# Optimization experiments

Measured on AMD Instinct MI355X. Metric: run time of the kernel, lower is better.

Reference implementation:

```python
import jax, jax.numpy as jnp
import numpy as np

B = 16384      # number of batched 6-node FC graphs
A = 6          # num_agents (nodes per graph)
D_OBS = 128    # raw observation dim
D_EMB = 250    # embedding / GAT feature dim
H = 3          # GAT heads (head outputs averaged to keep dim 250)
HID = 256
N_ACT = 5
NEG_SLOPE = 0.2


def setup_inputs() -> dict:
    key = jax.random.key(0)
    ks = jax.random.split(key, 16)
    def w(i, shape, scale=0.05):
        return jax.random.normal(ks[i], shape, dtype=jnp.float32) * scale
    return {
        "x": jax.random.normal(ks[0], (B * A, D_OBS), dtype=jnp.float32),
        "W_emb": w(1, (D_OBS, D_EMB)), "b_emb": jnp.zeros((D_EMB,), jnp.float32),
        "W_gat": w(2, (H, D_EMB, D_EMB)),
        "a_l": w(3, (H, D_EMB)), "a_r": w(4, (H, D_EMB)),
        "W1": w(5, (2 * D_EMB, HID)), "b1": jnp.zeros((HID,), jnp.float32),
        "W2": w(6, (HID, N_ACT)), "b2": jnp.zeros((N_ACT,), jnp.float32),
        "V1": w(7, (2 * D_EMB, HID)), "vb1": jnp.zeros((HID,), jnp.float32),
        "V2": w(8, (HID, 1)), "vb2": jnp.zeros((1,), jnp.float32),
    }


def reference(x, W_emb, b_emb, W_gat, a_l, a_r, W1, b1, W2, b2, V1, vb1, V2, vb2):
    # embedding layer
    h = jax.nn.relu(x @ W_emb + b_emb)                       # [N, 250]
    hb = h.reshape(B, A, D_EMB)                              # [B, 6, 250]
    # GAT on fully-connected 6-node graphs (incl. self edges), dense-masked form
    Wh = jnp.einsum("bad,hde->bhae", hb, W_gat)              # [B, H, 6, 250]
    el = jnp.einsum("bhae,he->bha", Wh, a_l)                 # dst term
    er = jnp.einsum("bhae,he->bha", Wh, a_r)                 # src term
    e = jax.nn.leaky_relu(el[:, :, :, None] + er[:, :, None, :], NEG_SLOPE)  # [B,H,6,6]
    attn = jax.nn.softmax(e, axis=-1)                        # edge softmax over neighbors
    gat = jnp.einsum("bhij,bhje->bhie", attn, Wh).mean(axis=1)  # mean over heads -> [B,6,250]
    feat = jnp.concatenate([hb, gat], axis=-1).reshape(B * A, 2 * D_EMB)  # [N, 500]
    # actor head (reg1)
    probs = jax.nn.softmax(jax.nn.relu(feat @ W1 + b1) @ W2 + b2, axis=-1)  # [N, 5]
    # critic head (reg2)
    value = jax.nn.relu(feat @ V1 + vb1) @ V2 + vb2           # [N, 1]
    return jnp.concatenate([probs, value], axis=-1)          # [N, 6]
```

## Files before the change

### kernel.cpp

```cpp
#include <hip/hip_runtime.h>

typedef unsigned short u16;
typedef unsigned int   u32;
typedef unsigned long long u64;
typedef __attribute__((ext_vector_type(4))) int   i32x4;
typedef __attribute__((ext_vector_type(4))) float f32x4;
typedef __attribute__((ext_vector_type(8))) short s16x8;

#define NROWS 98304L
#define LDF   512

__device__ __forceinline__ u16 f2bf(float x) {
  union { float f; u32 u; } v; v.f = x;
  return (u16)((v.u + 0x7FFFu + ((v.u >> 16) & 1u)) >> 16);
}
__device__ __forceinline__ float bf2f(u16 b) {
  union { float f; u32 u; } v; v.u = ((u32)b) << 16;
  return v.f;
}

__device__ __forceinline__ void gload_lds16(const u16* g, u16* l) {
  __builtin_amdgcn_global_load_lds(
      (const __attribute__((address_space(1))) unsigned int*)g,
      (__attribute__((address_space(3))) unsigned int*)l, 16, 0, 0);
}

__global__ __launch_bounds__(256)
void prep_weights(const float* __restrict__ W_emb, const float* __restrict__ b_emb,
                  const float* __restrict__ W_gat, const float* __restrict__ a_l,
                  const float* __restrict__ a_r, const float* __restrict__ W1,
                  const float* __restrict__ b1, const float* __restrict__ V1,
                  const float* __restrict__ vb1,
                  u16* __restrict__ Wemb_t, u16* __restrict__ Wgat_t,
                  u16* __restrict__ W1V1_t, float* __restrict__ bembp,
                  float* __restrict__ b1vb1)
{
  const int idx = blockIdx.x * 256 + threadIdx.x;
  const int stride = gridDim.x * 256;
  for (int t = idx; t < 256 * 128; t += stride) {
    int n = t >> 7, k = t & 127;
    Wemb_t[t] = f2bf(n < 250 ? W_emb[k * 250 + n] : 0.f);
  }
  for (int t = idx; t < 3 * 256 * 256; t += stride) {
    int h = t >> 16, rem = t & 65535, e = rem >> 8, d = rem & 255;
    float v = 0.f;
    if (e < 250 && d < 250) {
      v = W_gat[(h * 250 + d) * 250 + e];
    } else if ((e == 250 || e == 251) && d < 250) {
      const float* av = ((e == 250) ? a_l : a_r) + h * 250;
      const float* wrow = W_gat + ((long)h * 250 + d) * 250;
      float s = 0.f;
      for (int q = 0; q < 250; q++) s += wrow[q] * av[q];
      v = s;
    }
    Wgat_t[t] = f2bf(v);
  }
  for (int t = idx; t < 512 * 512; t += stride) {
    int n = t >> 9, k = t & 511;
    const float* src = (n < 256) ? W1 : V1;
    int col = n & 255;
    float v = 0.f;
    if (k < 250) v = src[k * 256 + col];
    else if (k >= 256 && k < 506) v = src[(k - 6) * 256 + col];
    W1V1_t[t] = f2bf(v);
  }
  for (int t = idx; t < 512; t += stride) b1vb1[t] = (t < 256) ? b1[t] : vb1[t - 256];
  for (int t = idx; t < 256; t += stride) bembp[t] = (t < 250) ? b_emb[t] : 0.f;
}

__global__ __launch_bounds__(256)
void cvt_x(const float* __restrict__ x, u16* __restrict__ xb)
{
  const long n = NROWS * 128;
  long i = ((long)blockIdx.x * 256 + threadIdx.x) * 8;
  const long stride = (long)gridDim.x * 256 * 8;
  for (; i < n; i += stride) {
    f32x4 a = *(const f32x4*)(x + i);
    f32x4 b = *(const f32x4*)(x + i + 4);
    i32x4 o;
    o[0] = (int)((u32)f2bf(a[0]) | ((u32)f2bf(a[1]) << 16));
    o[1] = (int)((u32)f2bf(a[2]) | ((u32)f2bf(a[3]) << 16));
    o[2] = (int)((u32)f2bf(b[0]) | ((u32)f2bf(b[1]) << 16));
    o[3] = (int)((u32)f2bf(b[2]) | ((u32)f2bf(b[3]) << 16));
    *(i32x4*)(xb + i) = o;
  }
}

template<int KSTEPS, int EPI>
__global__ __launch_bounds__(256, 2)
void gemm_bf16(const u16* __restrict__ A, int lda,
               const u16* __restrict__ B, int ldb, long strideB,
               u16* __restrict__ C, int ldc, long strideC,
               const float* __restrict__ bias)
{
  __shared__ __align__(16) u16 At[128 * 64];
  __shared__ __align__(16) u16 Bt[128 * 64];
  const int tid = threadIdx.x;
  const int w = tid >> 6, lane = tid & 63;
  const int fl = lane & 15, fh = lane >> 4;
  const int wr = (w >> 1) * 64, wc = (w & 1) * 64;
  const int srow = lane >> 3;
  const int scol = (((lane & 7) ^ srow) << 3);
  const int swz = (fl & 7) << 3;

  const u16* Ab = A + (long)blockIdx.x * 128 * lda;
  const u16* Bb = B + (long)blockIdx.z * strideB + (long)blockIdx.y * 128 * ldb;
  u16* Cb = C + (long)blockIdx.z * strideC + (long)blockIdx.x * 128 * ldc + blockIdx.y * 128;
  const float* biasb = bias + blockIdx.y * 128;

  f32x4 acc[4][4];
  #pragma unroll
  for (int m = 0; m < 4; m++)
    #pragma unroll
    for (int n = 0; n < 4; n++)
      acc[m][n] = f32x4{0.f, 0.f, 0.f, 0.f};

  for (int ks = 0; ks < KSTEPS; ks++) {
    __syncthreads();
    #pragma unroll
    for (int c = 0; c < 4; c++) {
      const int row = w * 32 + c * 8 + srow;
      gload_lds16(Ab + (long)row * lda + ks * 64 + scol, At + (w * 4 + c) * 512);
      gload_lds16(Bb + (long)row * ldb + ks * 64 + scol, Bt + (w * 4 + c) * 512);
    }
    __syncthreads();
    #pragma unroll
    for (int kk = 0; kk < 2; kk++) {
      s16x8 af[4], bfr[4];
      #pragma unroll
      for (int m = 0; m < 4; m++)
        af[m] = *(const s16x8*)(At + (wr + m * 16 + fl) * 64 + ((kk * 32 + fh * 8) ^ swz));
      #pragma unroll
      for (int n = 0; n < 4; n++)
        bfr[n] = *(const s16x8*)(Bt + (wc + n * 16 + fl) * 64 + ((kk * 32 + fh * 8) ^ swz));
      #pragma unroll
      for (int m = 0; m < 4; m++)
        #pragma unroll
        for (int n = 0; n < 4; n++)
          acc[m][n] = __builtin_amdgcn_mfma_f32_16x16x32_bf16(af[m], bfr[n], acc[m][n], 0, 0, 0);
    }
  }
  #pragma unroll
  for (int m = 0; m < 4; m++) {
    const int r0 = wr + m * 16 + fh * 4;
    #pragma unroll
    for (int n = 0; n < 4; n++) {
      const int col = wc + n * 16 + fl;
      float bvv = 0.f;
      if constexpr (EPI == 1) bvv = biasb[col];
      f32x4 v = acc[m][n];
      #pragma unroll
      for (int r = 0; r < 4; r++) {
        float xv = v[r];
        if constexpr (EPI == 1) xv = fmaxf(xv + bvv, 0.f);
        Cb[(long)(r0 + r) * ldc + col] = f2bf(xv);
      }
    }
  }
}

__global__ __launch_bounds__(256)
void attn_gat(const u16* __restrict__ Wh, u16* __restrict__ feat)
{
  const int w = threadIdx.x >> 6, lane = threadIdx.x & 63;
  const long g = (long)blockIdx.x * 4 + w;
  const int c0 = lane * 4;

  u64 raw[3][6];
  #pragma unroll
  for (int h = 0; h < 3; h++)
    #pragma unroll
    for (int i = 0; i < 6; i++)
      raw[h][i] = *(const u64*)(Wh + (((long)h * NROWS + g * 6 + i) << 8) + c0);

  float gacc[6][4];
  #pragma unroll
  for (int i = 0; i < 6; i++)
    #pragma unroll
    for (int q = 0; q < 4; q++) gacc[i][q] = 0.f;

  #pragma unroll
  for (int h = 0; h < 3; h++) {
    float whf[6][4];
    #pragma unroll
    for (int i = 0; i < 6; i++) {
      u64 v = raw[h][i];
      whf[i][0] = bf2f((u16)v);
      whf[i][1] = bf2f((u16)(v >> 16));
      whf[i][2] = bf2f((u16)(v >> 32));
      whf[i][3] = bf2f((u16)(v >> 48));
    }
    float el[6], er[6];
    #pragma unroll
    for (int i = 0; i < 6; i++) {
      el[i] = __shfl(whf[i][2], 62, 64);
      er[i] = __shfl(whf[i][3], 62, 64);
    }
    #pragma unroll
    for (int i = 0; i < 6; i++) {
      float e[6]; float mx = -1e30f;
      #pragma unroll
      for (int j = 0; j < 6; j++) {
        float t = el[i] + er[j];
        t = (t > 0.f) ? t : 0.2f * t;
        e[j] = t; mx = fmaxf(mx, t);
      }
      float s = 0.f;
      #pragma unroll
      for (int j = 0; j < 6; j++) { e[j] = __expf(e[j] - mx); s += e[j]; }
      float inv = 1.f / s;
      #pragma unroll
      for (int j = 0; j < 6; j++) {
        float a = e[j] * inv;
        #pragma unroll
        for (int q = 0; q < 4; q++) gacc[i][q] += a * whf[j][q];
      }
    }
  }
  #pragma unroll
  for (int i = 0; i < 6; i++) {
    const float k = 1.f / 3.f;
    u64 o = (u64)f2bf(gacc[i][0] * k)
          | ((u64)f2bf(gacc[i][1] * k) << 16)
          | ((u64)f2bf(gacc[i][2] * k) << 32)
          | ((u64)f2bf(gacc[i][3] * k) << 48);
    *(u64*)(feat + (g * 6 + i) * LDF + 256 + c0) = o;
  }
}

__global__ __launch_bounds__(256)
void heads(const u16* __restrict__ hidden, const float* __restrict__ W2,
           const float* __restrict__ b2, const float* __restrict__ V2,
           const float* __restrict__ vb2, float* __restrict__ out)
{
  const int w = threadIdx.x >> 6, lane = threadIdx.x & 63;
  const bool actor = lane < 32;
  const int kb = (lane & 31) * 8;
  float wreg[40];
  if (actor) {
    #pragma unroll
    for (int i = 0; i < 8; i++)
      #pragma unroll
      for (int j = 0; j < 5; j++) wreg[i * 5 + j] = W2[(kb + i) * 5 + j];
  } else {
    #pragma unroll
    for (int i = 0; i < 8; i++) wreg[i] = V2[kb + i];
  }
  float b2v[5];
  #pragma unroll
  for (int j = 0; j < 5; j++) b2v[j] = b2[j];
  const float vb2v = vb2[0];

  const long base = ((long)blockIdx.x * 4 + w) * 6;
  for (int rr = 0; rr < 6; ++rr) {
    const long row = base + rr;
    const u16* hp = hidden + row * 512 + (actor ? kb : 256 + kb);
    i32x4 hv4 = *(const i32x4*)hp;
    float hv[8];
    #pragma unroll
    for (int q = 0; q < 4; q++) {
      u32 u = (u32)hv4[q];
      hv[2 * q]     = bf2f((u16)u);
      hv[2 * q + 1] = bf2f((u16)(u >> 16));
    }
    float p[6] = {0.f, 0.f, 0.f, 0.f, 0.f, 0.f};
    if (actor) {
      #pragma unroll
      for (int j = 0; j < 5; j++) {
        float s = 0.f;
        #pragma unroll
        for (int i = 0; i < 8; i++) s += hv[i] * wreg[i * 5 + j];
        p[j] = s;
      }
    } else {
      float s = 0.f;
      #pragma unroll
      for (int i = 0; i < 8; i++) s += hv[i] * wreg[i];
      p[5] = s;
    }
    #pragma unroll
    for (int off = 1; off < 64; off <<= 1)
      #pragma unroll
      for (int j = 0; j < 6; j++) p[j] += __shfl_xor(p[j], off, 64);
    if (lane < 6) {
      float val;
      if (lane < 5) {
        float lg[5]; float mx = -1e30f;
        #pragma unroll
        for (int j = 0; j < 5; j++) { lg[j] = p[j] + b2v[j]; mx = fmaxf(mx, lg[j]); }
        float s = 0.f;
        #pragma unroll
        for (int j = 0; j < 5; j++) s += __expf(lg[j] - mx);
        val = __expf(lg[lane] - mx) / s;
      } else {
        val = p[5] + vb2v;
      }
      out[row * 6 + lane] = val;
    }
  }
}

extern "C" void kernel_launch(void* const* d_in, const int* in_sizes, int n_in,
                              void* d_out, int out_size, void* d_ws, size_t ws_size,
                              hipStream_t stream)
{
  const float* x     = (const float*)d_in[0];
  const float* W_emb = (const float*)d_in[1];
  const float* b_emb = (const float*)d_in[2];
  const float* W_gat = (const float*)d_in[3];
  const float* a_l   = (const float*)d_in[4];
  const float* a_r   = (const float*)d_in[5];
  const float* W1    = (const float*)d_in[6];
  const float* b1    = (const float*)d_in[7];
  const float* W2    = (const float*)d_in[8];
  const float* b2    = (const float*)d_in[9];
  const float* V1    = (const float*)d_in[10];
  const float* vb1   = (const float*)d_in[11];
  const float* V2    = (const float*)d_in[12];
  const float* vb2   = (const float*)d_in[13];

  char* ws = (char*)d_ws;
  u16* feat = (u16*)ws;
  char* r2  = ws + 100663296L;
  u16* xb   = (u16*)r2;
  u16* Whb  = (u16*)r2;
  u16* hid  = (u16*)r2;
  char* wt  = r2 + 150994944L;
  u16*   Wemb_t = (u16*)wt;
  u16*   Wgat_t = (u16*)(wt + 65536);
  u16*   W1V1_t = (u16*)(wt + 458752);
  float* b1vb1  = (float*)(wt + 983040);
  float* bembp  = (float*)(wt + 985088);

  prep_weights<<<256, 256, 0, stream>>>(W_emb, b_emb, W_gat, a_l, a_r, W1, b1, V1, vb1,
                                        Wemb_t, Wgat_t, W1V1_t, bembp, b1vb1);
  cvt_x<<<2048, 256, 0, stream>>>(x, xb);
  gemm_bf16<2, 1><<<dim3(768, 2, 1), 256, 0, stream>>>(xb, 128, Wemb_t, 128, 0L,
                                                       feat, 512, 0L, bembp);
  gemm_bf16<4, 0><<<dim3(768, 2, 3), 256, 0, stream>>>(feat, 512, Wgat_t, 256, 65536L,
                                                       Whb, 256, 25165824L, bembp);
  attn_gat<<<4096, 256, 0, stream>>>(Whb, feat);
  gemm_bf16<8, 1><<<dim3(768, 4, 1), 256, 0, stream>>>(feat, 512, W1V1_t, 512, 0L,
                                                       hid, 512, 0L, b1vb1);
  heads<<<4096, 256, 0, stream>>>(hid, W2, b2, V2, vb2, (float*)d_out);
}
```

Measured before the change: 390.3 us.

## Fuse actor/critic hidden GEMM with output heads and reorder GEMM grid

Replaces the third GEMM plus the separate heads kernel with one 1024-thread kernel. Each block computes the full 512-wide hidden layer for 128 rows, applies bias and ReLU, reduces against W2/V2 in registers and LDS, then writes the softmax probabilities and value directly. This removes the bf16 hidden-activation round trip through global memory and one launch. Separately, the other GEMMs put the N/head tiles on blockIdx.x so blocks sharing an A tile are scheduled together for better L2 reuse. The fused kernel uses large LDS and 1024-thread blocks, which may limit occupancy, and loads only a single buffered K tile per step.

```diff
diff --git a/kernel.cpp b/kernel.cpp
--- a/kernel.cpp
+++ b/kernel.cpp
@@ -91,7 +91,7 @@
 void gemm_bf16(const u16* __restrict__ A, int lda,
                const u16* __restrict__ B, int ldb, long strideB,
                u16* __restrict__ C, int ldc, long strideC,
-               const float* __restrict__ bias)
+               const float* __restrict__ bias, int nb)
 {
   __shared__ __align__(16) u16 At[128 * 64];
   __shared__ __align__(16) u16 Bt[128 * 64];
@@ -103,10 +103,14 @@
   const int scol = (((lane & 7) ^ srow) << 3);
   const int swz = (fl & 7) << 3;
 
-  const u16* Ab = A + (long)blockIdx.x * 128 * lda;
-  const u16* Bb = B + (long)blockIdx.z * strideB + (long)blockIdx.y * 128 * ldb;
-  u16* Cb = C + (long)blockIdx.z * strideC + (long)blockIdx.x * 128 * ldc + blockIdx.y * 128;
-  const float* biasb = bias + blockIdx.y * 128;
+  const int nidx = blockIdx.x % nb;
+  const int zidx = blockIdx.x / nb;
+  const int midx = blockIdx.y;
+
+  const u16* Ab = A + (long)midx * 128 * lda;
+  const u16* Bb = B + (long)zidx * strideB + (long)nidx * 128 * ldb;
+  u16* Cb = C + (long)zidx * strideC + (long)midx * 128 * ldc + nidx * 128;
+  const float* biasb = bias + nidx * 128;
 
   f32x4 acc[4][4];
   #pragma unroll
@@ -156,6 +160,152 @@
         Cb[(long)(r0 + r) * ldc + col] = f2bf(xv);
       }
     }
+  }
+}
+
+__global__ __launch_bounds__(1024, 2)
+void gemm3_heads(const u16* __restrict__ A,
+                 const u16* __restrict__ B,
+                 const float* __restrict__ b1vb1,
+                 const float* __restrict__ W2,
+                 const float* __restrict__ b2,
+                 const float* __restrict__ V2,
+                 const float* __restrict__ vb2,
+                 float* __restrict__ out)
+{
+  __shared__ __align__(16) u16 At[128 * 64];
+  __shared__ __align__(16) u16 Bt[512 * 64];
+  __shared__ float pstage[8][128][6];
+  const int tid = threadIdx.x;
+  const int w = tid >> 6, lane = tid & 63;
+  const int fl = lane & 15, fh = lane >> 4;
+  const int wrow = w >> 3, wcol = w & 7;
+  const int srow = lane >> 3;
+  const int schunk = (((lane & 7) ^ srow) << 3);
+  const int swz = (fl & 7) << 3;
+
+  const u16* Ab = A + (long)blockIdx.x * 128 * 512;
+
+  f32x4 acc[4][4];
+  #pragma unroll
+  for (int m = 0; m < 4; m++)
+    #pragma unroll
+    for (int n = 0; n < 4; n++)
+      acc[m][n] = f32x4{0.f, 0.f, 0.f, 0.f};
+
+  for (int ks = 0; ks < 8; ks++) {
+    __syncthreads();
+    gload_lds16(Ab + (long)(w * 8 + srow) * 512 + ks * 64 + schunk, At + w * 512);
+    #pragma unroll
+    for (int p = 0; p < 4; p++)
+      gload_lds16(B + (long)(p * 128 + w * 8 + srow) * 512 + ks * 64 + schunk,
+                  Bt + p * 8192 + w * 512);
+    __syncthreads();
+    #pragma unroll
+    for (int kk = 0; kk < 2; kk++) {
+      s16x8 af[4], bfr[4];
+      #pragma unroll
+      for (int m = 0; m < 4; m++)
+        af[m] = *(const s16x8*)(At + (wrow * 64 + m * 16 + fl) * 64 + ((kk * 32 + fh * 8) ^ swz));
+      #pragma unroll
+      for (int n = 0; n < 4; n++)
+        bfr[n] = *(const s16x8*)(Bt + (wcol * 64 + n * 16 + fl) * 64 + ((kk * 32 + fh * 8) ^ swz));
+      #pragma unroll
+      for (int m = 0; m < 4; m++)
+        #pragma unroll
+        for (int n = 0; n < 4; n++)
+          acc[m][n] = __builtin_amdgcn_mfma_f32_16x16x32_bf16(af[m], bfr[n], acc[m][n], 0, 0, 0);
+    }
+  }
+
+  float bv[4];
+  #pragma unroll
+  for (int n = 0; n < 4; n++) bv[n] = b1vb1[wcol * 64 + n * 16 + fl];
+
+  if (wcol < 4) {
+    #pragma unroll
+    for (int m = 0; m < 4; m++) {
+      float ps[4][5];
+      #pragma unroll
+      for (int r = 0; r < 4; r++)
+        #pragma unroll
+        for (int j = 0; j < 5; j++) ps[r][j] = 0.f;
+      #pragma unroll
+      for (int n = 0; n < 4; n++) {
+        const int col = wcol * 64 + n * 16 + fl;
+        const float* w2c = W2 + col * 5;
+        float w2r[5];
+        #pragma unroll
+        for (int j = 0; j < 5; j++) w2r[j] = w2c[j];
+        #pragma unroll
+        for (int r = 0; r < 4; r++) {
+          float hid = fmaxf(acc[m][n][r] + bv[n], 0.f);
+          #pragma unroll
+          for (int j = 0; j < 5; j++) ps[r][j] += hid * w2r[j];
+        }
+      }
+      #pragma unroll
+      for (int off = 1; off < 16; off <<= 1)
+        #pragma unroll
+        for (int r = 0; r < 4; r++)
+          #pragma unroll
+          for (int j = 0; j < 5; j++) ps[r][j] += __shfl_xor(ps[r][j], off, 16);
+      if (fl == 0) {
+        const int row = wrow * 64 + m * 16 + fh * 4;
+        #pragma unroll
+        for (int r = 0; r < 4; r++)
+          #pragma unroll
+          for (int j = 0; j < 5; j++) pstage[wcol][row + r][j] = ps[r][j];
+      }
+    }
+  } else {
+    #pragma unroll
+    for (int m = 0; m < 4; m++) {
+      float ps[4];
+      #pragma unroll
+      for (int r = 0; r < 4; r++) ps[r] = 0.f;
+      #pragma unroll
+      for (int n = 0; n < 4; n++) {
+        const int col = wcol * 64 + n * 16 + fl;
+        const float v2c = V2[col - 256];
+        #pragma unroll
+        for (int r = 0; r < 4; r++) {
+          float hid = fmaxf(acc[m][n][r] + bv[n], 0.f);
+          ps[r] += hid * v2c;
+        }
+      }
+      #pragma unroll
+      for (int off = 1; off < 16; off <<= 1)
+        #pragma unroll
+        for (int r = 0; r < 4; r++) ps[r] += __shfl_xor(ps[r], off, 16);
+      if (fl == 0) {
+        const int row = wrow * 64 + m * 16 + fh * 4;
+        #pragma unroll
+        for (int r = 0; r < 4; r++) pstage[wcol][row + r][5] = ps[r];
+      }
+    }
+  }
+  __syncthreads();
+
+  if (tid < 128) {
+    float lg[5];
+    #pragma unroll
+    for (int j = 0; j < 5; j++)
+      lg[j] = pstage[0][tid][j] + pstage[1][tid][j] + pstage[2][tid][j] +
+              pstage[3][tid][j] + b2[j];
+    float val = pstage[4][tid][5] + pstage[5][tid][5] + pstage[6][tid][5] +
+                pstage[7][tid][5] + vb2[0];
+    float mx = -1e30f;
+    #pragma unroll
+    for (int j = 0; j < 5; j++) mx = fmaxf(mx, lg[j]);
+    float s = 0.f, e[5];
+    #pragma unroll
+    for (int j = 0; j < 5; j++) { e[j] = __expf(lg[j] - mx); s += e[j]; }
+    float inv = 1.f / s;
+    float* op = out + ((long)blockIdx.x * 128 + tid) * 6;
+    #pragma unroll
+    for (int j = 0; j < 5; j++) op[j] = e[j] * inv;
+    op[5] = val;
   }
 }
 
@@ -225,78 +375,6 @@
           | ((u64)f2bf(gacc[i][2] * k) << 32)
           | ((u64)f2bf(gacc[i][3] * k) << 48);
     *(u64*)(feat + (g * 6 + i) * LDF + 256 + c0) = o;
-  }
-}
-
-__global__ __launch_bounds__(256)
-void heads(const u16* __restrict__ hidden, const float* __restrict__ W2,
-           const float* __restrict__ b2, const float* __restrict__ V2,
-           const float* __restrict__ vb2, float* __restrict__ out)
-{
-  const int w = threadIdx.x >> 6, lane = threadIdx.x & 63;
-  const bool actor = lane < 32;
-  const int kb = (lane & 31) * 8;
-  float wreg[40];
-  if (actor) {
-    #pragma unroll
-    for (int i = 0; i < 8; i++)
-      #pragma unroll
-      for (int j = 0; j < 5; j++) wreg[i * 5 + j] = W2[(kb + i) * 5 + j];
-  } else {
-    #pragma unroll
-    for (int i = 0; i < 8; i++) wreg[i] = V2[kb + i];
-  }
-  float b2v[5];
-  #pragma unroll
-  for (int j = 0; j < 5; j++) b2v[j] = b2[j];
-  const float vb2v = vb2[0];
-
-  const long base = ((long)blockIdx.x * 4 + w) * 6;
-  for (int rr = 0; rr < 6; ++rr) {
-    const long row = base + rr;
-    const u16* hp = hidden + row * 512 + (actor ? kb : 256 + kb);
-    i32x4 hv4 = *(const i32x4*)hp;
-    float hv[8];
-    #pragma unroll
-    for (int q = 0; q < 4; q++) {
-      u32 u = (u32)hv4[q];
-      hv[2 * q]     = bf2f((u16)u);
-      hv[2 * q + 1] = bf2f((u16)(u >> 16));
-    }
-    float p[6] = {0.f, 0.f, 0.f, 0.f, 0.f, 0.f};
-    if (actor) {
-      #pragma unroll
-      for (int j = 0; j < 5; j++) {
-        float s = 0.f;
-        #pragma unroll
-        for (int i = 0; i < 8; i++) s += hv[i] * wreg[i * 5 + j];
-        p[j] = s;
-      }
-    } else {
-      float s = 0.f;
-      #pragma unroll
-      for (int i = 0; i < 8; i++) s += hv[i] * wreg[i];
-      p[5] = s;
-    }
-    #pragma unroll
-    for (int off = 1; off < 64; off <<= 1)
-      #pragma unroll
-      for (int j = 0; j < 6; j++) p[j] += __shfl_xor(p[j], off, 64);
-    if (lane < 6) {
-      float val;
-      if (lane < 5) {
-        float lg[5]; float mx = -1e30f;
-        #pragma unroll
-        for (int j = 0; j < 5; j++) { lg[j] = p[j] + b2v[j]; mx = fmaxf(mx, lg[j]); }
-        float s = 0.f;
-        #pragma unroll
-        for (int j = 0; j < 5; j++) s += __expf(lg[j] - mx);
-        val = __expf(lg[lane] - mx) / s;
-      } else {
-        val = p[5] + vb2v;
-      }
-      out[row * 6 + lane] = val;
-    }
   }
 }
 
@@ -324,7 +402,6 @@
   char* r2  = ws + 100663296L;
   u16* xb   = (u16*)r2;
   u16* Whb  = (u16*)r2;
-  u16* hid  = (u16*)r2;
   char* wt  = r2 + 150994944L;
   u16*   Wemb_t = (u16*)wt;
   u16*   Wgat_t = (u16*)(wt + 65536);
@@ -335,12 +412,11 @@
   prep_weights<<<256, 256, 0, stream>>>(W_emb, b_emb, W_gat, a_l, a_r, W1, b1, V1, vb1,
                                         Wemb_t, Wgat_t, W1V1_t, bembp, b1vb1);
   cvt_x<<<2048, 256, 0, stream>>>(x, xb);
-  gemm_bf16<2, 1><<<dim3(768, 2, 1), 256, 0, stream>>>(xb, 128, Wemb_t, 128, 0L,
-                                                       feat, 512, 0L, bembp);
-  gemm_bf16<4, 0><<<dim3(768, 2, 3), 256, 0, stream>>>(feat, 512, Wgat_t, 256, 65536L,
-                                                       Whb, 256, 25165824L, bembp);
+  gemm_bf16<2, 1><<<dim3(2, 768), 256, 0, stream>>>(xb, 128, Wemb_t, 128, 0L,
+                                                    feat, 512, 0L, bembp, 2);
+  gemm_bf16<4, 0><<<dim3(6, 768), 256, 0, stream>>>(feat, 512, Wgat_t, 256, 65536L,
+                                                    Whb, 256, 25165824L, bembp, 2);
   attn_gat<<<4096, 256, 0, stream>>>(Whb, feat);
-  gemm_bf16<8, 1><<<dim3(768, 4, 1), 256, 0, stream>>>(feat, 512, W1V1_t, 512, 0L,
-                                                       hid, 512, 0L, b1vb1);
-  heads<<<4096, 256, 0, stream>>>(hid, W2, b2, V2, vb2, (float*)d_out);
-}
+  gemm3_heads<<<768, 1024, 0, stream>>>(feat, W1V1_t, b1vb1, W2, b2, V2, vb2,
+                                        (float*)d_out);
+}
```

Result: faster. 364.4 us (-6.6%).
